# Kernel optimization log

Measured on AMD Instinct MI355X. Metric: run time of the kernel, lower is better.

The kernel has to match this reference:

```python
import jax, jax.numpy as jnp
import numpy as np

B, C, H, W = 16, 64, 256, 256


def setup_inputs() -> dict:
    key = jax.random.key(0)
    ks = jax.random.split(key, 4)
    scale = 1.0 / np.sqrt(C)
    return {
        "x": jax.random.normal(ks[0], (B, C, H, W), dtype=jnp.float32),
        "g_w": jax.random.normal(ks[1], (C, C), dtype=jnp.float32) * scale,
        "g_b": jnp.zeros((C,), dtype=jnp.float32),
        "theta_w": jax.random.normal(ks[2], (C, C), dtype=jnp.float32) * scale,
        "theta_b": jnp.zeros((C,), dtype=jnp.float32),
        "phi_w": jax.random.normal(ks[3], (C, C), dtype=jnp.float32) * scale,
        "phi_b": jnp.zeros((C,), dtype=jnp.float32),
    }


def reference(x, g_w, g_b, theta_w, theta_b, phi_w, phi_b):
    b, c, h, w = x.shape
    hw = h * w
    xf = x.reshape(b, c, hw)  # [B, C, HW]

    def proj(wt, bs):
        # 1x1 conv == channel-mixing linear: out[b,o,n] = sum_c wt[o,c] * x[b,c,n] + bs[o]
        return jnp.einsum('oc,bcn->bon', wt, xf) + bs[None, :, None]

    g_y = jax.nn.softmax(proj(g_w, g_b), axis=1)              # softmax over channels
    theta_x = jax.nn.softmax(proj(theta_w, theta_b), axis=-1)  # softmax over HW
    phi_x = proj(phi_w, phi_b)

    # similarity = phi_x @ theta_x^T  -> [B, C, C]
    similarity = jnp.einsum('bcn,bdn->bcd', phi_x, theta_x)
    # attention = similarity @ g_y   -> [B, C, HW]
    attention = jnp.einsum('bcd,bdn->bcn', similarity, g_y).reshape(b, c, h, w)

    return jax.nn.leaky_relu(x + attention, negative_slope=0.1)
```

## Files before the change

kernel.cpp:

```cpp
#include <hip/hip_runtime.h>
#include <hip/hip_fp16.h>
#include <cstdint>
#include <cstddef>

#define BATCH 16
#define CH 64
#define HWN 65536
#define NBLK 64
#define NPAD 136
#define DPAD 72
#define ACHUNK 8

typedef __attribute__((ext_vector_type(8))) _Float16 half8;
typedef __attribute__((ext_vector_type(4))) float f32x4;

static const size_t SP_OFF = 0;
static const size_t ZP_OFF = SP_OFF + (size_t)BATCH * NBLK * 4096 * 4;
static const size_t M_OFF  = ZP_OFF + (size_t)BATCH * NBLK * 4 * 64 * 4;

__device__ __forceinline__ half8 load_frag_f32(const float* p) {
    const float4 w0 = *(const float4*)p;
    const float4 w1 = *(const float4*)(p + 4);
    half8 f;
    f[0] = (_Float16)w0.x; f[1] = (_Float16)w0.y;
    f[2] = (_Float16)w0.z; f[3] = (_Float16)w0.w;
    f[4] = (_Float16)w1.x; f[5] = (_Float16)w1.y;
    f[6] = (_Float16)w1.z; f[7] = (_Float16)w1.w;
    return f;
}

__global__ __launch_bounds__(256) void proj_s(
    const float* __restrict__ x,
    const float* __restrict__ thw, const float* __restrict__ thb,
    const float* __restrict__ phw, const float* __restrict__ phb,
    float* __restrict__ Sp, float* __restrict__ Zp)
{
    __shared__ ushort El[64 * NPAD];
    __shared__ ushort Pl[64 * NPAD];
    const int b   = blockIdx.y;
    const int blk = blockIdx.x;
    const int tid = threadIdx.x;
    const int wid = tid >> 6;
    const int l   = tid & 63;
    const int lr  = l & 15;
    const int lg  = l >> 4;

    half8 Wf[2][4][2];
#pragma unroll
    for (int p = 0; p < 2; p++) {
        const float* wsrc = p ? phw : thw;
#pragma unroll
        for (int ot = 0; ot < 4; ot++)
#pragma unroll
            for (int g = 0; g < 2; g++)
                Wf[p][ot][g] = load_frag_f32(wsrc + (ot * 16 + lr) * 64 + g * 32 + lg * 8);
    }
    float bT[16], bP[16];
#pragma unroll
    for (int ot = 0; ot < 4; ot++)
#pragma unroll
        for (int i = 0; i < 4; i++) {
            bT[ot * 4 + i] = thb[ot * 16 + lg * 4 + i];
            bP[ot * 4 + i] = phb[ot * 16 + lg * 4 + i];
        }

    f32x4 Sacc[4];
#pragma unroll
    for (int j = 0; j < 4; j++) Sacc[j] = (f32x4){0.f, 0.f, 0.f, 0.f};
    float z[16];
#pragma unroll
    for (int k = 0; k < 16; k++) z[k] = 0.f;

    const float* xb = x + (size_t)b * CH * HWN;

    for (int chk = 0; chk < 8; chk++) {
        const int nb = blk * 1024 + chk * 128;
#pragma unroll
        for (int nt = 0; nt < 2; nt++) {
            const int ncol = wid * 32 + nt * 16 + lr;
            const float* xp = xb + (nb + ncol);
            half8 xf0, xf1;
#pragma unroll
            for (int i = 0; i < 8; i++) xf0[i] = (_Float16)xp[(size_t)(lg * 8 + i) * HWN];
#pragma unroll
            for (int i = 0; i < 8; i++) xf1[i] = (_Float16)xp[(size_t)(32 + lg * 8 + i) * HWN];
#pragma unroll
            for (int ot = 0; ot < 4; ot++) {
                const int off = (ot * 16 + lg * 4) * NPAD + ncol;
                f32x4 acc = {bT[ot * 4 + 0], bT[ot * 4 + 1], bT[ot * 4 + 2], bT[ot * 4 + 3]};
                acc = __builtin_amdgcn_mfma_f32_16x16x32_f16(Wf[0][ot][0], xf0, acc, 0, 0, 0);
                acc = __builtin_amdgcn_mfma_f32_16x16x32_f16(Wf[0][ot][1], xf1, acc, 0, 0, 0);
#pragma unroll
                for (int i = 0; i < 4; i++) {
                    float e = __expf(acc[i]);
                    z[ot * 4 + i] += e;
                    El[off + i * NPAD] = __half_as_ushort(__float2half(e));
                }
                f32x4 pcc = {bP[ot * 4 + 0], bP[ot * 4 + 1], bP[ot * 4 + 2], bP[ot * 4 + 3]};
                pcc = __builtin_amdgcn_mfma_f32_16x16x32_f16(Wf[1][ot][0], xf0, pcc, 0, 0, 0);
                pcc = __builtin_amdgcn_mfma_f32_16x16x32_f16(Wf[1][ot][1], xf1, pcc, 0, 0, 0);
#pragma unroll
                for (int i = 0; i < 4; i++)
                    Pl[off + i * NPAD] = __half_as_ushort(__float2half(pcc[i]));
            }
        }
        __syncthreads();
        const ushort* arow = Pl + (wid * 16 + lr) * NPAD;
#pragma unroll
        for (int g = 0; g < 4; g++) {
            const int coff = g * 32 + lg * 8;
            half8 af = *(const half8*)(arow + coff);
#pragma unroll
            for (int j = 0; j < 4; j++) {
                half8 bf = *(const half8*)(El + (j * 16 + lr) * NPAD + coff);
                Sacc[j] = __builtin_amdgcn_mfma_f32_16x16x32_f16(af, bf, Sacc[j], 0, 0, 0);
            }
        }
        __syncthreads();
    }

    float* sp = Sp + (size_t)(b * NBLK + blk) * 4096;
#pragma unroll
    for (int j = 0; j < 4; j++)
#pragma unroll
        for (int i = 0; i < 4; i++)
            sp[(wid * 16 + lg * 4 + i) * 64 + j * 16 + lr] = Sacc[j][i];

#pragma unroll
    for (int k = 0; k < 16; k++) {
        float v = z[k];
        v += __shfl_xor(v, 1, 64);
        v += __shfl_xor(v, 2, 64);
        v += __shfl_xor(v, 4, 64);
        v += __shfl_xor(v, 8, 64);
        z[k] = v;
    }
    if (lr == 0) {
        float* zp = Zp + ((size_t)(b * NBLK + blk) * 4 + wid) * 64;
#pragma unroll
        for (int t = 0; t < 4; t++)
#pragma unroll
            for (int i = 0; i < 4; i++)
                zp[t * 16 + lg * 4 + i] = z[t * 4 + i];
    }
}

__global__ __launch_bounds__(256) void normalize_S(
    const float* __restrict__ Sp, const float* __restrict__ Zp,
    float* __restrict__ M)
{
    const int b   = blockIdx.x;
    const int tid = threadIdx.x;
    __shared__ float Zl[64];
    if (tid < 64) {
        float s = 0.f;
        const float* zp = Zp + (size_t)b * (NBLK * 4) * 64 + tid;
        for (int k = 0; k < NBLK * 4; k++) s += zp[(size_t)k * 64];
        Zl[tid] = 1.0f / s;
    }
    __syncthreads();
    const float* sp = Sp + (size_t)b * NBLK * 4096;
    float* mp = M + (size_t)b * 4096;
    for (int idx = tid; idx < 4096; idx += 256) {
        float s = 0.f;
        for (int k = 0; k < NBLK; k++) s += sp[(size_t)k * 4096 + idx];
        mp[idx] = s * Zl[idx & 63];
    }
}

__global__ __launch_bounds__(256) void attn_mfma(
    const float* __restrict__ x,
    const float* __restrict__ gw, const float* __restrict__ gb,
    const float* __restrict__ M,
    float* __restrict__ out)
{
    __shared__ ushort El[128 * DPAD];
    const int b   = blockIdx.y;
    const int tid = threadIdx.x;
    const int wid = tid >> 6;
    const int l   = tid & 63;
    const int lr  = l & 15;
    const int lg  = l >> 4;

    const float* xb = x + (size_t)b * CH * HWN;
    float* outb = out + (size_t)b * CH * HWN;

    half8 Gf[4][2];
#pragma unroll
    for (int ot = 0; ot < 4; ot++)
#pragma unroll
        for (int kg = 0; kg < 2; kg++)
            Gf[ot][kg] = load_frag_f32(gw + (ot * 16 + lr) * 64 + kg * 32 + lg * 8);
    float bG[16];
#pragma unroll
    for (int ot = 0; ot < 4; ot++)
#pragma unroll
        for (int i = 0; i < 4; i++) bG[ot * 4 + i] = gb[ot * 16 + lg * 4 + i];

    half8 Mf[4][2];
    const float* Mb = M + (size_t)b * 4096;
#pragma unroll
    for (int ct = 0; ct < 4; ct++)
#pragma unroll
        for (int kg = 0; kg < 2; kg++)
            Mf[ct][kg] = load_frag_f32(Mb + (ct * 16 + lr) * 64 + kg * 32 + lg * 8);

    for (int chk = 0; chk < ACHUNK; chk++) {
        const int nb = blockIdx.x * (128 * ACHUNK) + chk * 128;
        float rz[2];

#pragma unroll
        for (int nt = 0; nt < 2; nt++) {
            const int ncol = wid * 32 + nt * 16 + lr;
            const float* xp = xb + nb + ncol;
            half8 xf0, xf1;
#pragma unroll
            for (int i = 0; i < 8; i++) xf0[i] = (_Float16)xp[(size_t)(lg * 8 + i) * HWN];
#pragma unroll
            for (int i = 0; i < 8; i++) xf1[i] = (_Float16)xp[(size_t)(32 + lg * 8 + i) * HWN];

            float gy[4][4];
#pragma unroll
            for (int ot = 0; ot < 4; ot++) {
                f32x4 acc = {bG[ot * 4 + 0], bG[ot * 4 + 1], bG[ot * 4 + 2], bG[ot * 4 + 3]};
                acc = __builtin_amdgcn_mfma_f32_16x16x32_f16(Gf[ot][0], xf0, acc, 0, 0, 0);
                acc = __builtin_amdgcn_mfma_f32_16x16x32_f16(Gf[ot][1], xf1, acc, 0, 0, 0);
#pragma unroll
                for (int i = 0; i < 4; i++) gy[ot][i] = acc[i];
            }
            float m = gy[0][0];
#pragma unroll
            for (int ot = 0; ot < 4; ot++)
#pragma unroll
                for (int i = 0; i < 4; i++) m = fmaxf(m, gy[ot][i]);
            m = fmaxf(m, __shfl_xor(m, 16, 64));
            m = fmaxf(m, __shfl_xor(m, 32, 64));

            float zs = 0.f;
            ushort* erow = El + ncol * DPAD;
#pragma unroll
            for (int ot = 0; ot < 4; ot++) {
                float e0 = __expf(gy[ot][0] - m);
                float e1 = __expf(gy[ot][1] - m);
                float e2 = __expf(gy[ot][2] - m);
                float e3 = __expf(gy[ot][3] - m);
                zs += e0 + e1 + e2 + e3;
                uint2 pk;
                pk.x = (uint)__half_as_ushort(__float2half(e0)) |
                       ((uint)__half_as_ushort(__float2half(e1)) << 16);
                pk.y = (uint)__half_as_ushort(__float2half(e2)) |
                       ((uint)__half_as_ushort(__float2half(e3)) << 16);
                *(uint2*)(erow + ot * 16 + lg * 4) = pk;
            }
            zs += __shfl_xor(zs, 16, 64);
            zs += __shfl_xor(zs, 32, 64);
            rz[nt] = 1.0f / zs;
        }
        __syncthreads();

#pragma unroll
        for (int nt = 0; nt < 2; nt++) {
            const int ncol = wid * 32 + nt * 16 + lr;
            const ushort* brow = El + ncol * DPAD;
            half8 bf0 = *(const half8*)(brow + lg * 8);
            half8 bf1 = *(const half8*)(brow + 32 + lg * 8);
            const float sc = rz[nt];
#pragma unroll
            for (int ct = 0; ct < 4; ct++) {
                f32x4 acc = {0.f, 0.f, 0.f, 0.f};
                acc = __builtin_amdgcn_mfma_f32_16x16x32_f16(Mf[ct][0], bf0, acc, 0, 0, 0);
                acc = __builtin_amdgcn_mfma_f32_16x16x32_f16(Mf[ct][1], bf1, acc, 0, 0, 0);
#pragma unroll
                for (int i = 0; i < 4; i++) {
                    const size_t off = (size_t)(ct * 16 + lg * 4 + i) * HWN + nb + ncol;
                    float v = xb[off] + acc[i] * sc;
                    outb[off] = (v >= 0.f) ? v : 0.1f * v;
                }
            }
        }
        __syncthreads();
    }
}

extern "C" void kernel_launch(void* const* d_in, const int* in_sizes, int n_in,
                              void* d_out, int out_size, void* d_ws, size_t ws_size,
                              hipStream_t stream)
{
    const float* x   = (const float*)d_in[0];
    const float* gw  = (const float*)d_in[1];
    const float* gb  = (const float*)d_in[2];
    const float* thw = (const float*)d_in[3];
    const float* thb = (const float*)d_in[4];
    const float* phw = (const float*)d_in[5];
    const float* phb = (const float*)d_in[6];
    float* out = (float*)d_out;

    char* ws = (char*)d_ws;
    float* Sp = (float*)(ws + SP_OFF);
    float* Zp = (float*)(ws + ZP_OFF);
    float* M  = (float*)(ws + M_OFF);

    dim3 blk(256);
    proj_s<<<dim3(NBLK, BATCH), blk, 0, stream>>>(x, thw, thb, phw, phb, Sp, Zp);
    normalize_S<<<dim3(BATCH), blk, 0, stream>>>(Sp, Zp, M);
    attn_mfma<<<dim3(HWN / (128 * ACHUNK), BATCH), blk, 0, stream>>>(x, gw, gb, M, out);
}
```

Before: 300.0 us.

## Stage attention output through LDS for coalesced float4 residual stores; split normalize

The attention kernel now writes its MFMA results into a padded shared-memory tile. All threads then read the residual x and write the output as contiguous float4 vectors, replacing the scattered per-element global accesses. Column assignment across waves is reordered so each 64-column half is covered by all four waves. The normalize kernel is split over 8 slices per batch so it launches 128 blocks instead of 16. The price is extra LDS usage, more barriers per chunk, and a redundant Z reduction in every slice.

```diff
diff --git a/kernel.cpp b/kernel.cpp
--- a/kernel.cpp
+++ b/kernel.cpp
@@ -9,6 +9,7 @@
 #define NBLK 64
 #define NPAD 136
 #define DPAD 72
+#define TPAD 68
 #define ACHUNK 8
 
 typedef __attribute__((ext_vector_type(8))) _Float16 half8;
@@ -149,7 +150,8 @@
     const float* __restrict__ Sp, const float* __restrict__ Zp,
     float* __restrict__ M)
 {
-    const int b   = blockIdx.x;
+    const int b   = blockIdx.y;
+    const int sl  = blockIdx.x;
     const int tid = threadIdx.x;
     __shared__ float Zl[64];
     if (tid < 64) {
@@ -161,7 +163,9 @@
     __syncthreads();
     const float* sp = Sp + (size_t)b * NBLK * 4096;
     float* mp = M + (size_t)b * 4096;
-    for (int idx = tid; idx < 4096; idx += 256) {
+#pragma unroll
+    for (int h = 0; h < 2; h++) {
+        const int idx = sl * 512 + h * 256 + tid;
         float s = 0.f;
         for (int k = 0; k < NBLK; k++) s += sp[(size_t)k * 4096 + idx];
         mp[idx] = s * Zl[idx & 63];
@@ -174,7 +178,8 @@
     const float* __restrict__ M,
     float* __restrict__ out)
 {
-    __shared__ ushort El[128 * DPAD];
+    __shared__ __align__(16) ushort El[128 * DPAD];
+    __shared__ __align__(16) float  Tl[64 * TPAD];
     const int b   = blockIdx.y;
     const int tid = threadIdx.x;
     const int wid = tid >> 6;
@@ -211,7 +216,7 @@
 
 #pragma unroll
         for (int nt = 0; nt < 2; nt++) {
-            const int ncol = wid * 32 + nt * 16 + lr;
+            const int ncol = nt * 64 + wid * 16 + lr;
             const float* xp = xb + nb + ncol;
             half8 xf0, xf1;
 #pragma unroll
@@ -256,14 +261,14 @@
             zs += __shfl_xor(zs, 32, 64);
             rz[nt] = 1.0f / zs;
         }
-        __syncthreads();
 
 #pragma unroll
         for (int nt = 0; nt < 2; nt++) {
-            const int ncol = wid * 32 + nt * 16 + lr;
+            const int ncol = nt * 64 + wid * 16 + lr;
             const ushort* brow = El + ncol * DPAD;
             half8 bf0 = *(const half8*)(brow + lg * 8);
             half8 bf1 = *(const half8*)(brow + 32 + lg * 8);
+            __syncthreads();
             const float sc = rz[nt];
 #pragma unroll
             for (int ct = 0; ct < 4; ct++) {
@@ -271,14 +276,26 @@
                 acc = __builtin_amdgcn_mfma_f32_16x16x32_f16(Mf[ct][0], bf0, acc, 0, 0, 0);
                 acc = __builtin_amdgcn_mfma_f32_16x16x32_f16(Mf[ct][1], bf1, acc, 0, 0, 0);
 #pragma unroll
-                for (int i = 0; i < 4; i++) {
-                    const size_t off = (size_t)(ct * 16 + lg * 4 + i) * HWN + nb + ncol;
-                    float v = xb[off] + acc[i] * sc;
-                    outb[off] = (v >= 0.f) ? v : 0.1f * v;
-                }
-            }
-        }
-        __syncthreads();
+                for (int i = 0; i < 4; i++)
+                    Tl[(ct * 16 + lg * 4 + i) * TPAD + wid * 16 + lr] = acc[i] * sc;
+            }
+            __syncthreads();
+#pragma unroll
+            for (int it = 0; it < 4; it++) {
+                const int ch = (tid >> 4) + it * 16;
+                const int p  = (tid & 15) * 4;
+                const float4 a = *(const float4*)&Tl[ch * TPAD + p];
+                const size_t go = (size_t)ch * HWN + nb + nt * 64 + p;
+                const float4 xv = *(const float4*)(xb + go);
+                float4 o;
+                float v0 = xv.x + a.x, v1 = xv.y + a.y, v2 = xv.z + a.z, v3 = xv.w + a.w;
+                o.x = (v0 >= 0.f) ? v0 : 0.1f * v0;
+                o.y = (v1 >= 0.f) ? v1 : 0.1f * v1;
+                o.z = (v2 >= 0.f) ? v2 : 0.1f * v2;
+                o.w = (v3 >= 0.f) ? v3 : 0.1f * v3;
+                *(float4*)(outb + go) = o;
+            }
+        }
     }
 }
 
@@ -302,6 +319,6 @@
 
     dim3 blk(256);
     proj_s<<<dim3(NBLK, BATCH), blk, 0, stream>>>(x, thw, thb, phw, phb, Sp, Zp);
-    normalize_S<<<dim3(BATCH), blk, 0, stream>>>(Sp, Zp, M);
+    normalize_S<<<dim3(8, BATCH), blk, 0, stream>>>(Sp, Zp, M);
     attn_mfma<<<dim3(HWN / (128 * ACHUNK), BATCH), blk, 0, stream>>>(x, gw, gb, M, out);
 }
```

Result: faster. 289.9 us (-3.4%).

## Stage x through an LDS transpose with float4 loads and parallelize S normalization

Applied to the files above, without the earlier changes.

Both the projection kernel and the attention kernel now load x with coalesced float4 reads per channel row. Each value is converted to fp16 and written transposed into a padded shared-memory tile, and the MFMA fragments are then read from that tile. Before, each lane made eight strided scalar global loads per fragment. The projection kernel now works in 64-column chunks, and one barrier in each kernel is removed where the data stays within a wave. normalize_S is split across 8 blocks per batch for more parallelism. The cost is extra LDS traffic, possible bank conflicts on the transposed 16-bit stores, and an added barrier per chunk.

```diff
diff --git a/kernel.cpp b/kernel.cpp
--- a/kernel.cpp
+++ b/kernel.cpp
@@ -7,8 +7,7 @@
 #define CH 64
 #define HWN 65536
 #define NBLK 64
-#define NPAD 136
-#define DPAD 72
+#define PAD 72
 #define ACHUNK 8
 
 typedef __attribute__((ext_vector_type(8))) _Float16 half8;
@@ -35,8 +34,9 @@
     const float* __restrict__ phw, const float* __restrict__ phb,
     float* __restrict__ Sp, float* __restrict__ Zp)
 {
-    __shared__ ushort El[64 * NPAD];
-    __shared__ ushort Pl[64 * NPAD];
+    __shared__ __align__(16) ushort xt[64 * PAD];
+    __shared__ __align__(16) ushort El[64 * PAD];
+    __shared__ __align__(16) ushort Pl[64 * PAD];
     const int b   = blockIdx.y;
     const int blk = blockIdx.x;
     const int tid = threadIdx.x;
@@ -72,51 +72,58 @@
     for (int k = 0; k < 16; k++) z[k] = 0.f;
 
     const float* xb = x + (size_t)b * CH * HWN;
-
-    for (int chk = 0; chk < 8; chk++) {
-        const int nb = blk * 1024 + chk * 128;
-#pragma unroll
-        for (int nt = 0; nt < 2; nt++) {
-            const int ncol = wid * 32 + nt * 16 + lr;
-            const float* xp = xb + (nb + ncol);
-            half8 xf0, xf1;
-#pragma unroll
-            for (int i = 0; i < 8; i++) xf0[i] = (_Float16)xp[(size_t)(lg * 8 + i) * HWN];
-#pragma unroll
-            for (int i = 0; i < 8; i++) xf1[i] = (_Float16)xp[(size_t)(32 + lg * 8 + i) * HWN];
-#pragma unroll
-            for (int ot = 0; ot < 4; ot++) {
-                const int off = (ot * 16 + lg * 4) * NPAD + ncol;
-                f32x4 acc = {bT[ot * 4 + 0], bT[ot * 4 + 1], bT[ot * 4 + 2], bT[ot * 4 + 3]};
-                acc = __builtin_amdgcn_mfma_f32_16x16x32_f16(Wf[0][ot][0], xf0, acc, 0, 0, 0);
-                acc = __builtin_amdgcn_mfma_f32_16x16x32_f16(Wf[0][ot][1], xf1, acc, 0, 0, 0);
-#pragma unroll
-                for (int i = 0; i < 4; i++) {
-                    float e = __expf(acc[i]);
-                    z[ot * 4 + i] += e;
-                    El[off + i * NPAD] = __half_as_ushort(__float2half(e));
-                }
-                f32x4 pcc = {bP[ot * 4 + 0], bP[ot * 4 + 1], bP[ot * 4 + 2], bP[ot * 4 + 3]};
-                pcc = __builtin_amdgcn_mfma_f32_16x16x32_f16(Wf[1][ot][0], xf0, pcc, 0, 0, 0);
-                pcc = __builtin_amdgcn_mfma_f32_16x16x32_f16(Wf[1][ot][1], xf1, pcc, 0, 0, 0);
-#pragma unroll
-                for (int i = 0; i < 4; i++)
-                    Pl[off + i * NPAD] = __half_as_ushort(__float2half(pcc[i]));
-            }
+    const int sch = tid >> 4;
+    const int spx = (tid & 15) * 4;
+
+    for (int chk = 0; chk < 16; chk++) {
+        const int nb = blk * 1024 + chk * 64;
+
+#pragma unroll
+        for (int it = 0; it < 4; it++) {
+            const int ch = sch + it * 16;
+            const float4 v = *(const float4*)(xb + (size_t)ch * HWN + nb + spx);
+            xt[(spx + 0) * PAD + ch] = __half_as_ushort(__float2half(v.x));
+            xt[(spx + 1) * PAD + ch] = __half_as_ushort(__float2half(v.y));
+            xt[(spx + 2) * PAD + ch] = __half_as_ushort(__float2half(v.z));
+            xt[(spx + 3) * PAD + ch] = __half_as_ushort(__float2half(v.w));
         }
         __syncthreads();
-        const ushort* arow = Pl + (wid * 16 + lr) * NPAD;
-#pragma unroll
-        for (int g = 0; g < 4; g++) {
+
+        const int ncol = wid * 16 + lr;
+        half8 xf0 = *(const half8*)(xt + ncol * PAD + lg * 8);
+        half8 xf1 = *(const half8*)(xt + ncol * PAD + 32 + lg * 8);
+#pragma unroll
+        for (int ot = 0; ot < 4; ot++) {
+            const int off = (ot * 16 + lg * 4) * PAD + ncol;
+            f32x4 acc = {bT[ot * 4 + 0], bT[ot * 4 + 1], bT[ot * 4 + 2], bT[ot * 4 + 3]};
+            acc = __builtin_amdgcn_mfma_f32_16x16x32_f16(Wf[0][ot][0], xf0, acc, 0, 0, 0);
+            acc = __builtin_amdgcn_mfma_f32_16x16x32_f16(Wf[0][ot][1], xf1, acc, 0, 0, 0);
+#pragma unroll
+            for (int i = 0; i < 4; i++) {
+                float e = __expf(acc[i]);
+                z[ot * 4 + i] += e;
+                El[off + i * PAD] = __half_as_ushort(__float2half(e));
+            }
+            f32x4 pcc = {bP[ot * 4 + 0], bP[ot * 4 + 1], bP[ot * 4 + 2], bP[ot * 4 + 3]};
+            pcc = __builtin_amdgcn_mfma_f32_16x16x32_f16(Wf[1][ot][0], xf0, pcc, 0, 0, 0);
+            pcc = __builtin_amdgcn_mfma_f32_16x16x32_f16(Wf[1][ot][1], xf1, pcc, 0, 0, 0);
+#pragma unroll
+            for (int i = 0; i < 4; i++)
+                Pl[off + i * PAD] = __half_as_ushort(__float2half(pcc[i]));
+        }
+        __syncthreads();
+
+        const ushort* arow = Pl + (wid * 16 + lr) * PAD;
+#pragma unroll
+        for (int g = 0; g < 2; g++) {
             const int coff = g * 32 + lg * 8;
             half8 af = *(const half8*)(arow + coff);
 #pragma unroll
             for (int j = 0; j < 4; j++) {
-                half8 bf = *(const half8*)(El + (j * 16 + lr) * NPAD + coff);
+                half8 bf = *(const half8*)(El + (j * 16 + lr) * PAD + coff);
                 Sacc[j] = __builtin_amdgcn_mfma_f32_16x16x32_f16(af, bf, Sacc[j], 0, 0, 0);
             }
         }
-        __syncthreads();
     }
 
     float* sp = Sp + (size_t)(b * NBLK + blk) * 4096;
@@ -149,7 +156,8 @@
     const float* __restrict__ Sp, const float* __restrict__ Zp,
     float* __restrict__ M)
 {
-    const int b   = blockIdx.x;
+    const int b   = blockIdx.y;
+    const int sl  = blockIdx.x;
     const int tid = threadIdx.x;
     __shared__ float Zl[64];
     if (tid < 64) {
@@ -161,7 +169,9 @@
     __syncthreads();
     const float* sp = Sp + (size_t)b * NBLK * 4096;
     float* mp = M + (size_t)b * 4096;
-    for (int idx = tid; idx < 4096; idx += 256) {
+#pragma unroll
+    for (int h = 0; h < 2; h++) {
+        const int idx = sl * 512 + h * 256 + tid;
         float s = 0.f;
         for (int k = 0; k < NBLK; k++) s += sp[(size_t)k * 4096 + idx];
         mp[idx] = s * Zl[idx & 63];
@@ -174,7 +184,8 @@
     const float* __restrict__ M,
     float* __restrict__ out)
 {
-    __shared__ ushort El[128 * DPAD];
+    __shared__ __align__(16) ushort xt[128 * PAD];
+    __shared__ __align__(16) ushort El[128 * PAD];
     const int b   = blockIdx.y;
     const int tid = threadIdx.x;
     const int wid = tid >> 6;
@@ -205,19 +216,29 @@
         for (int kg = 0; kg < 2; kg++)
             Mf[ct][kg] = load_frag_f32(Mb + (ct * 16 + lr) * 64 + kg * 32 + lg * 8);
 
+    const int sch = tid >> 5;
+    const int spx = (tid & 31) * 4;
+
     for (int chk = 0; chk < ACHUNK; chk++) {
         const int nb = blockIdx.x * (128 * ACHUNK) + chk * 128;
+
+#pragma unroll
+        for (int it = 0; it < 8; it++) {
+            const int ch = sch + it * 8;
+            const float4 v = *(const float4*)(xb + (size_t)ch * HWN + nb + spx);
+            xt[(spx + 0) * PAD + ch] = __half_as_ushort(__float2half(v.x));
+            xt[(spx + 1) * PAD + ch] = __half_as_ushort(__float2half(v.y));
+            xt[(spx + 2) * PAD + ch] = __half_as_ushort(__float2half(v.z));
+            xt[(spx + 3) * PAD + ch] = __half_as_ushort(__float2half(v.w));
+        }
+        __syncthreads();
+
         float rz[2];
-
 #pragma unroll
         for (int nt = 0; nt < 2; nt++) {
             const int ncol = wid * 32 + nt * 16 + lr;
-            const float* xp = xb + nb + ncol;
-            half8 xf0, xf1;
-#pragma unroll
-            for (int i = 0; i < 8; i++) xf0[i] = (_Float16)xp[(size_t)(lg * 8 + i) * HWN];
-#pragma unroll
-            for (int i = 0; i < 8; i++) xf1[i] = (_Float16)xp[(size_t)(32 + lg * 8 + i) * HWN];
+            half8 xf0 = *(const half8*)(xt + ncol * PAD + lg * 8);
+            half8 xf1 = *(const half8*)(xt + ncol * PAD + 32 + lg * 8);
 
             float gy[4][4];
 #pragma unroll
@@ -237,7 +258,7 @@
             m = fmaxf(m, __shfl_xor(m, 32, 64));
 
             float zs = 0.f;
-            ushort* erow = El + ncol * DPAD;
+            ushort* erow = El + ncol * PAD;
 #pragma unroll
             for (int ot = 0; ot < 4; ot++) {
                 float e0 = __expf(gy[ot][0] - m);
@@ -256,12 +277,11 @@
             zs += __shfl_xor(zs, 32, 64);
             rz[nt] = 1.0f / zs;
         }
-        __syncthreads();
 
 #pragma unroll
         for (int nt = 0; nt < 2; nt++) {
             const int ncol = wid * 32 + nt * 16 + lr;
-            const ushort* brow = El + ncol * DPAD;
+            const ushort* brow = El + ncol * PAD;
             half8 bf0 = *(const half8*)(brow + lg * 8);
             half8 bf1 = *(const half8*)(brow + 32 + lg * 8);
             const float sc = rz[nt];
@@ -302,6 +322,6 @@
 
     dim3 blk(256);
     proj_s<<<dim3(NBLK, BATCH), blk, 0, stream>>>(x, thw, thb, phw, phb, Sp, Zp);
-    normalize_S<<<dim3(BATCH), blk, 0, stream>>>(Sp, Zp, M);
+    normalize_S<<<dim3(8, BATCH), blk, 0, stream>>>(Sp, Zp, M);
     attn_mfma<<<dim3(HWN / (128 * ACHUNK), BATCH), blk, 0, stream>>>(x, gw, gb, M, out);
 }
```

After: 262.8 us. 12.4% less time.
